# Performance work log

Hardware: AMD Instinct MI355X
Metric: run time of the kernel (lower is better)

The kernel has to match this reference:

```python
import jax, jax.numpy as jnp
import numpy as np

D = 512      # dgm / hidden width
L = 3        # n_dgm_layers
B = 131072   # collocation batch
SCALE = 0.02 # init scale to keep gates unsaturated


def setup_inputs() -> dict:
    key = jax.random.key(0)
    ks = jax.random.split(key, 12)
    X = jax.random.normal(ks[0], (B, 2), jnp.float32)
    t = jax.random.uniform(ks[1], (B, 1), jnp.float32)
    # input layer: Linear(3, D)
    W_in = jax.random.normal(ks[2], (3, D), jnp.float32) * SCALE
    b_in = jnp.zeros((D,), jnp.float32)
    # dense hidden: Linear(D, D)
    W_h1 = jax.random.normal(ks[3], (D, D), jnp.float32) * SCALE
    b_h1 = jnp.zeros((D,), jnp.float32)
    # projection to dgm dims: Linear(D, D)
    W_hd = jax.random.normal(ks[4], (D, D), jnp.float32) * SCALE
    b_hd = jnp.zeros((D,), jnp.float32)
    # DGM layers: 12 linears each, order [Uz,Wz,Bz, Ug,Wg,Bg, Ur,Wr,Br, Uh,Wh,Bh]
    dgm_W = jax.random.normal(ks[5], (L, 12, D, D), jnp.float32) * SCALE
    dgm_b = jnp.zeros((L, 12, D), jnp.float32)
    # output head: Linear(D, 1)
    W_out = jax.random.normal(ks[6], (D, 1), jnp.float32) * SCALE
    b_out = jnp.zeros((1,), jnp.float32)
    return {"X": X, "t": t, "W_in": W_in, "b_in": b_in, "W_h1": W_h1,
            "b_h1": b_h1, "W_hd": W_hd, "b_hd": b_hd, "dgm_W": dgm_W,
            "dgm_b": dgm_b, "W_out": W_out, "b_out": b_out}


def reference(X, t, W_in, b_in, W_h1, b_h1, W_hd, b_hd, dgm_W, dgm_b, W_out, b_out):
    inp = jnp.concatenate([X, t], axis=1)          # [B, 3]
    x = jnp.tanh(inp @ W_in + b_in)                # input layer + tanh
    x = jnp.tanh(x @ W_h1 + b_h1)                  # hidden Linear + tanh
    x = x @ W_hd + b_hd                            # hidden -> dgm projection (no act)
    S1 = x
    S = x
    for l in range(L):                             # small fixed layer loop
        W = dgm_W[l]
        b = dgm_b[l]
        lin = lambda i, v: v @ W[i] + b[i]
        Z = jax.nn.sigmoid(lin(0, x) + lin(1, S) + lin(2, S1))
        G = jax.nn.sigmoid(lin(3, x) + lin(4, S1) + lin(5, S))
        R = jax.nn.sigmoid(lin(6, x) + lin(7, S) + lin(8, S1))
        H = jnp.tanh(lin(9, x) + lin(10, S * R) + lin(11, S1))
        S = (1.0 - G) * H + Z * S
    return S @ W_out + b_out                       # [B, 1]
```

## Files before the change

### kernel.cpp

```cpp
#include <hip/hip_runtime.h>
#include <stdint.h>

namespace {

constexpr int B_ROWS = 131072;

typedef __attribute__((ext_vector_type(8))) short bf16x8;
typedef __attribute__((ext_vector_type(4))) float f32x4;

__device__ __forceinline__ unsigned short f2bf(float f) {
  unsigned u = __builtin_bit_cast(unsigned, f);
  u += 0x7fffu + ((u >> 16) & 1u);
  return (unsigned short)(u >> 16);
}
__device__ __forceinline__ float bf2f(unsigned short h) {
  unsigned u = ((unsigned)h) << 16;
  return __builtin_bit_cast(float, u);
}
__device__ __forceinline__ float sigm(float v) { return 1.0f / (1.0f + __expf(-v)); }


__global__ void pack_t_k(const float* __restrict__ W, unsigned short* __restrict__ Wt) {
  int idx = blockIdx.x * 256 + threadIdx.x;
  int n = idx >> 9, k = idx & 511;
  Wt[idx] = f2bf(W[(k << 9) + n]);
}

__global__ void pack_zgr_k(const float* __restrict__ dgmW, unsigned short* __restrict__ Wt) {
  long idx = (long)blockIdx.x * 256 + threadIdx.x;
  int l = (int)(idx / (1536 * 1024));
  int rest = (int)(idx - (long)l * (1536 * 1024));
  int n = rest >> 10, k = rest & 1023;
  int g = n >> 9, nn = n & 511;
  const int xi0[3] = {0, 3, 6};
  const int xi1[3] = {2, 4, 8};
  const int si[3] = {1, 5, 7};
  float v;
  if (k < 512)
    v = dgmW[(((long)(l * 12 + xi0[g]) << 9) + k) * 512 + nn] +
        dgmW[(((long)(l * 12 + xi1[g]) << 9) + k) * 512 + nn];
  else
    v = dgmW[(((long)(l * 12 + si[g]) << 9) + (k - 512)) * 512 + nn];
  Wt[idx] = f2bf(v);
}

__global__ void pack_h_k(const float* __restrict__ dgmW, unsigned short* __restrict__ Wt) {
  long idx = (long)blockIdx.x * 256 + threadIdx.x;
  int l = (int)(idx / (512 * 1024));
  int rest = (int)(idx - (long)l * (512 * 1024));
  int n = rest >> 10, k = rest & 1023;
  float v;
  if (k < 512)
    v = dgmW[(((long)(l * 12 + 9) << 9) + k) * 512 + n] +
        dgmW[(((long)(l * 12 + 11) << 9) + k) * 512 + n];
  else
    v = dgmW[(((long)(l * 12 + 10) << 9) + (k - 512)) * 512 + n];
  Wt[idx] = f2bf(v);
}

__global__ void pack_bias_k(const float* __restrict__ dgmb, float* __restrict__ bzgr,
                            float* __restrict__ bh) {
  int idx = blockIdx.x * 256 + threadIdx.x;
  if (idx >= 3 * 2048) return;
  int l = idx >> 11, n = idx & 2047;
  const float* bl = dgmb + l * 12 * 512;
  if (n < 1536) {
    int g = n >> 9, nn = n & 511;
    bzgr[l * 1536 + n] =
        bl[(g * 3 + 0) * 512 + nn] + bl[(g * 3 + 1) * 512 + nn] + bl[(g * 3 + 2) * 512 + nn];
  } else {
    int nn = n - 1536;
    bh[l * 512 + nn] = bl[9 * 512 + nn] + bl[10 * 512 + nn] + bl[11 * 512 + nn];
  }
}

__global__ void front0_k(const float* __restrict__ X, const float* __restrict__ t,
                         const float* __restrict__ Win, const float* __restrict__ bin,
                         unsigned short* __restrict__ x0, long row0) {
  long idx = (long)blockIdx.x * 256 + threadIdx.x;
  long r = idx >> 9;
  int c = (int)(idx & 511);
  long gr = row0 + r;
  float a = X[gr * 2] * Win[c] + X[gr * 2 + 1] * Win[512 + c] + t[gr] * Win[1024 + c] + bin[c];
  x0[idx] = f2bf(tanhf(a));
}

__global__ void head_k(const unsigned short* __restrict__ S, const float* __restrict__ Wout,
                       const float* __restrict__ bout, float* __restrict__ out, long row0) {
  const int lane = threadIdx.x & 63, wid = threadIdx.x >> 6;
  const long r = (long)blockIdx.x * 4 + wid;
  bf16x8 sv = *(const bf16x8*)&S[r * 512 + lane * 8];
  float sum = 0.f;
#pragma unroll
  for (int i = 0; i < 8; ++i) sum += bf2f((unsigned short)sv[i]) * Wout[lane * 8 + i];
#pragma unroll
  for (int off = 32; off > 0; off >>= 1) sum += __shfl_down(sum, off);
  if (lane == 0) out[row0 + r] = sum + bout[0];
}

template <int EPI, int KTILES>
__global__ __launch_bounds__(256, 2) void gemm_k(
    const unsigned short* __restrict__ a0, const unsigned short* __restrict__ a1,
    const unsigned short* __restrict__ wt, const float* __restrict__ bias,
    unsigned short* __restrict__ o0, unsigned short* __restrict__ o1,
    unsigned short* __restrict__ o2, const unsigned short* __restrict__ e0,
    const unsigned short* __restrict__ e1) {
  constexpr int K = KTILES * 64;
  __shared__ __align__(16) unsigned short As[128 * 64];
  __shared__ __align__(16) unsigned short Bs[128 * 64];
  const int tid = threadIdx.x;
  const int lane = tid & 63;
  const int wid = tid >> 6;
  const int wm = wid >> 1, wn = wid & 1;
  const long brow = (long)blockIdx.y * 128;
  const int bcol = blockIdx.x * 128;
  f32x4 acc[4][4] = {};

  for (int kt = 0; kt < KTILES; ++kt) {
    const unsigned short* asrc = (kt < 8) ? a0 : a1;
    const int kloc = (kt & 7) * 64;
    __syncthreads();
#pragma unroll
    for (int i = 0; i < 4; ++i) {
      const int c = tid + 256 * i;
      const int r = c >> 3, k8 = (c & 7) * 8;
      __builtin_amdgcn_global_load_lds(
          (const __attribute__((address_space(1))) void*)(asrc + (brow + r) * 512 + kloc + k8),
          (__attribute__((address_space(3))) void*)(&As[c * 8]), 16, 0, 0);
      __builtin_amdgcn_global_load_lds(
          (const __attribute__((address_space(1))) void*)(wt + (long)(bcol + r) * K + kt * 64 + k8),
          (__attribute__((address_space(3))) void*)(&Bs[c * 8]), 16, 0, 0);
    }
    __syncthreads();
#pragma unroll
    for (int ks = 0; ks < 2; ++ks) {
      bf16x8 af[4], bfv[4];
#pragma unroll
      for (int m = 0; m < 4; ++m)
        af[m] = *(const bf16x8*)&As[(wm * 64 + m * 16 + (lane & 15)) * 64 + ks * 32 + (lane >> 4) * 8];
#pragma unroll
      for (int n = 0; n < 4; ++n)
        bfv[n] = *(const bf16x8*)&Bs[(wn * 64 + n * 16 + (lane & 15)) * 64 + ks * 32 + (lane >> 4) * 8];
#pragma unroll
      for (int m = 0; m < 4; ++m)
#pragma unroll
        for (int n = 0; n < 4; ++n)
          acc[m][n] = __builtin_amdgcn_mfma_f32_16x16x32_bf16(af[m], bfv[n], acc[m][n], 0, 0, 0);
    }
  }

  const int g = bcol >> 9;
#pragma unroll
  for (int m = 0; m < 4; ++m) {
#pragma unroll
    for (int n = 0; n < 4; ++n) {
      const int col = bcol + wn * 64 + n * 16 + (lane & 15);
      const float bs = bias[col];
#pragma unroll
      for (int j = 0; j < 4; ++j) {
        const long row = brow + wm * 64 + m * 16 + (lane >> 4) * 4 + j;
        float v = acc[m][n][j] + bs;
        if constexpr (EPI == 0) {
          o0[row * 512 + col] = f2bf(tanhf(v));
        } else if constexpr (EPI == 1) {
          unsigned short b = f2bf(v);
          o0[row * 512 + col] = b;
          o1[row * 512 + col] = b;
        } else if constexpr (EPI == 2) {
          const int nn = col & 511;
          const float sgv = sigm(v);
          if (g == 0) {
            o0[row * 512 + nn] = f2bf(sgv * bf2f(e0[row * 512 + nn]));
          } else if (g == 1) {
            o1[row * 512 + nn] = f2bf(1.0f - sgv);
          } else {
            o2[row * 512 + nn] = f2bf(sgv * bf2f(e0[row * 512 + nn]));
          }
        } else {
          const float h = tanhf(v);
          const float omg = bf2f(e0[row * 512 + col]);
          const float zs = bf2f(e1[row * 512 + col]);
          o0[row * 512 + col] = f2bf(omg * h + zs);
        }
      }
    }
  }
}

}

extern "C" void kernel_launch(void* const* d_in, const int* in_sizes, int n_in,
                              void* d_out, int out_size, void* d_ws, size_t ws_size,
                              hipStream_t stream) {
  const float* X = (const float*)d_in[0];
  const float* t = (const float*)d_in[1];
  const float* W_in = (const float*)d_in[2];
  const float* b_in = (const float*)d_in[3];
  const float* W_h1 = (const float*)d_in[4];
  const float* b_h1 = (const float*)d_in[5];
  const float* W_hd = (const float*)d_in[6];
  const float* b_hd = (const float*)d_in[7];
  const float* dgm_W = (const float*)d_in[8];
  const float* dgm_b = (const float*)d_in[9];
  const float* W_out = (const float*)d_in[10];
  const float* b_out = (const float*)d_in[11];
  float* out = (float*)d_out;
  char* ws = (char*)d_ws;

  size_t off = 0;
  auto alloc = [&](size_t bytes) {
    size_t o = off;
    off = (off + bytes + 255) & ~(size_t)255;
    return o;
  };
  size_t o_wth1 = alloc((size_t)512 * 512 * 2);
  size_t o_wthd = alloc((size_t)512 * 512 * 2);
  size_t o_wtzgr = alloc((size_t)3 * 1536 * 1024 * 2);
  size_t o_wth = alloc((size_t)3 * 512 * 1024 * 2);
  size_t o_bzgr = alloc((size_t)3 * 1536 * 4);
  size_t o_bh = alloc((size_t)3 * 512 * 4);
  size_t actoff = off;

  unsigned short* wth1 = (unsigned short*)(ws + o_wth1);
  unsigned short* wthd = (unsigned short*)(ws + o_wthd);
  unsigned short* wtzgr = (unsigned short*)(ws + o_wtzgr);
  unsigned short* wth = (unsigned short*)(ws + o_wth);
  float* bzgr = (float*)(ws + o_bzgr);
  float* bh = (float*)(ws + o_bh);

  size_t avail = ws_size > actoff ? ws_size - actoff : 0;
  int nch = 1;
  while (nch < 1024 && (size_t)(B_ROWS / nch) * 512 * 2 * 5 > avail) nch <<= 1;
  const int R = B_ROWS / nch;
  unsigned short* xb = (unsigned short*)(ws + actoff);
  unsigned short* Sb = xb + (size_t)R * 512;
  unsigned short* ZSb = Sb + (size_t)R * 512;
  unsigned short* OGb = ZSb + (size_t)R * 512;
  unsigned short* SRb = OGb + (size_t)R * 512;

  pack_t_k<<<1024, 256, 0, stream>>>(W_h1, wth1);
  pack_t_k<<<1024, 256, 0, stream>>>(W_hd, wthd);
  pack_zgr_k<<<18432, 256, 0, stream>>>(dgm_W, wtzgr);
  pack_h_k<<<6144, 256, 0, stream>>>(dgm_W, wth);
  pack_bias_k<<<24, 256, 0, stream>>>(dgm_b, bzgr, bh);

  for (int c = 0; c < nch; ++c) {
    long row0 = (long)c * R;
    dim3 g4(4, R / 128), g12(12, R / 128);
    front0_k<<<R * 2, 256, 0, stream>>>(X, t, W_in, b_in, ZSb, row0);
    gemm_k<0, 8><<<g4, 256, 0, stream>>>(ZSb, nullptr, wth1, b_h1, OGb, nullptr, nullptr,
                                         nullptr, nullptr);
    gemm_k<1, 8><<<g4, 256, 0, stream>>>(OGb, nullptr, wthd, b_hd, xb, Sb, nullptr,
                                         nullptr, nullptr);
    for (int l = 0; l < 3; ++l) {
      gemm_k<2, 16><<<g12, 256, 0, stream>>>(xb, Sb, wtzgr + (size_t)l * 1536 * 1024,
                                             bzgr + l * 1536, ZSb, OGb, SRb, Sb, nullptr);
      gemm_k<3, 16><<<g4, 256, 0, stream>>>(xb, SRb, wth + (size_t)l * 512 * 1024,
                                            bh + l * 512, Sb, nullptr, nullptr, OGb, ZSb);
    }
    head_k<<<R / 4, 256, 0, stream>>>(Sb, W_out, b_out, out, row0);
  }
}
```

Baseline: 3.627 ms.

## Rewrite GEMM with 256x256 tiles, double-buffered swizzled LDS and XCD remap

Replaces the 128x128, 256-thread GEMM with a 512-thread kernel that computes 256x256 output tiles. It uses 128KB of dynamic LDS split into two buffers, so the next K-tile is prefetched while MFMAs run on the current one. LDS rows are XOR-swizzled to avoid bank conflicts, workgroups are remapped so neighbouring tiles land on the same XCD, and s_setprio is raised around the MFMA block. The larger tile raises arithmetic intensity per load, at the cost of one block per CU, heavy register use and a requirement that the chunk row count be a multiple of 256.

```diff
diff --git a/kernel.cpp b/kernel.cpp
--- a/kernel.cpp
+++ b/kernel.cpp
@@ -98,67 +98,107 @@
   if (lane == 0) out[row0 + r] = sum + bout[0];
 }
 
-template <int EPI, int KTILES>
-__global__ __launch_bounds__(256, 2) void gemm_k(
+#define GLD(gsrc, ldst)                                                      \
+  __builtin_amdgcn_global_load_lds(                                          \
+      (const __attribute__((address_space(1))) void*)(gsrc),                 \
+      (__attribute__((address_space(3))) void*)(ldst), 16, 0, 0)
+
+template <int EPI, int KT>
+__global__ __launch_bounds__(512, 2) void gemm2_k(
     const unsigned short* __restrict__ a0, const unsigned short* __restrict__ a1,
     const unsigned short* __restrict__ wt, const float* __restrict__ bias,
     unsigned short* __restrict__ o0, unsigned short* __restrict__ o1,
     unsigned short* __restrict__ o2, const unsigned short* __restrict__ e0,
     const unsigned short* __restrict__ e1) {
-  constexpr int K = KTILES * 64;
-  __shared__ __align__(16) unsigned short As[128 * 64];
-  __shared__ __align__(16) unsigned short Bs[128 * 64];
+  constexpr int K = KT * 64;
+  extern __shared__ unsigned short lds[];
   const int tid = threadIdx.x;
-  const int lane = tid & 63;
-  const int wid = tid >> 6;
-  const int wm = wid >> 1, wn = wid & 1;
-  const long brow = (long)blockIdx.y * 128;
-  const int bcol = blockIdx.x * 128;
-  f32x4 acc[4][4] = {};
-
-  for (int kt = 0; kt < KTILES; ++kt) {
-    const unsigned short* asrc = (kt < 8) ? a0 : a1;
-    const int kloc = (kt & 7) * 64;
+  const int lane = tid & 63, wid = tid >> 6;
+  const int wm = wid >> 2, wn = wid & 3;
+  const int lr = lane & 15, kk = lane >> 4;
+
+  const int gx = gridDim.x;
+  const int nwg = gx * (int)gridDim.y;
+  const int orig = (int)blockIdx.y * gx + (int)blockIdx.x;
+  const int q = nwg >> 3, rr = nwg & 7;
+  const int xcd = orig & 7, lo = orig >> 3;
+  const int wg = ((xcd < rr) ? xcd * (q + 1) : rr * (q + 1) + (xcd - rr) * q) + lo;
+  const long brow = (long)(wg / gx) * 256;
+  const int bcol = (wg % gx) * 256;
+
+  const int gp8 = ((kk ^ ((lr >> 1) & 3)) << 3);
+  const int a_rd = (wm * 128 + lr) * 32 + gp8;
+  const int b_rd = 16384 + (wn * 64 + lr) * 32 + gp8;
+  const int r0 = tid >> 2, gl0 = (tid & 3) ^ ((r0 >> 1) & 3);
+  const int c1t = tid + 512, r1 = c1t >> 2, gl1 = (c1t & 3) ^ ((r1 >> 1) & 3);
+  const int aL0 = r0 * 512 + gl0 * 8, aL1 = r1 * 512 + gl1 * 8;
+  const size_t bL0 = (size_t)r0 * K + gl0 * 8, bL1 = (size_t)r1 * K + gl1 * 8;
+  const int dL0 = tid * 8, dL1 = (tid + 512) * 8;
+
+  f32x4 acc[8][4] = {};
+  bf16x8 af[8], bf[4];
+
+  const long abase = brow * 512;
+  const size_t bbase = (size_t)bcol * K;
+
+  auto stA = [&](int kt, int ks, int dbo) {
+    const unsigned short* src = (KT == 16 && (kt & 8)) ? a1 : a0;
+    const long pb = abase + (kt & 7) * 64 + ks * 32;
+    const int d = dbo + ks * 8192;
+    GLD(src + pb + aL0, lds + d + dL0);
+    GLD(src + pb + aL1, lds + d + dL1);
+  };
+  auto stB = [&](int kt, int ks, int dbo) {
+    const size_t pb = bbase + kt * 64 + ks * 32;
+    const int d = dbo + 16384 + ks * 8192;
+    GLD(wt + pb + bL0, lds + d + dL0);
+    GLD(wt + pb + bL1, lds + d + dL1);
+  };
+
+  stA(0, 0, 0);
+  stB(0, 0, 0);
+  stA(0, 1, 0);
+  stB(0, 1, 0);
+  asm volatile("s_waitcnt vmcnt(0)" ::: "memory");
+  __syncthreads();
+
+  for (int t = 0; t < KT; ++t) {
+    const int cbo = (t & 1) << 15;
+    const int nbo = cbo ^ 32768;
+    if (t + 1 < KT) {
+      stA(t + 1, 0, nbo);
+      stB(t + 1, 0, nbo);
+      stA(t + 1, 1, nbo);
+      stB(t + 1, 1, nbo);
+    }
+#pragma unroll
+    for (int ks = 0; ks < 2; ++ks) {
+      const int ko = cbo + ks * 8192;
+#pragma unroll
+      for (int n = 0; n < 4; ++n) bf[n] = *(const bf16x8*)(lds + ko + b_rd + n * 512);
+#pragma unroll
+      for (int m = 0; m < 8; ++m) af[m] = *(const bf16x8*)(lds + ko + a_rd + m * 512);
+      __builtin_amdgcn_s_setprio(1);
+#pragma unroll
+      for (int m = 0; m < 8; ++m)
+#pragma unroll
+        for (int n = 0; n < 4; ++n)
+          acc[m][n] = __builtin_amdgcn_mfma_f32_16x16x32_bf16(af[m], bf[n], acc[m][n], 0, 0, 0);
+      __builtin_amdgcn_s_setprio(0);
+    }
+    asm volatile("s_waitcnt vmcnt(0)" ::: "memory");
     __syncthreads();
-#pragma unroll
-    for (int i = 0; i < 4; ++i) {
-      const int c = tid + 256 * i;
-      const int r = c >> 3, k8 = (c & 7) * 8;
-      __builtin_amdgcn_global_load_lds(
-          (const __attribute__((address_space(1))) void*)(asrc + (brow + r) * 512 + kloc + k8),
-          (__attribute__((address_space(3))) void*)(&As[c * 8]), 16, 0, 0);
-      __builtin_amdgcn_global_load_lds(
-          (const __attribute__((address_space(1))) void*)(wt + (long)(bcol + r) * K + kt * 64 + k8),
-          (__attribute__((address_space(3))) void*)(&Bs[c * 8]), 16, 0, 0);
-    }
-    __syncthreads();
-#pragma unroll
-    for (int ks = 0; ks < 2; ++ks) {
-      bf16x8 af[4], bfv[4];
-#pragma unroll
-      for (int m = 0; m < 4; ++m)
-        af[m] = *(const bf16x8*)&As[(wm * 64 + m * 16 + (lane & 15)) * 64 + ks * 32 + (lane >> 4) * 8];
-#pragma unroll
-      for (int n = 0; n < 4; ++n)
-        bfv[n] = *(const bf16x8*)&Bs[(wn * 64 + n * 16 + (lane & 15)) * 64 + ks * 32 + (lane >> 4) * 8];
-#pragma unroll
-      for (int m = 0; m < 4; ++m)
-#pragma unroll
-        for (int n = 0; n < 4; ++n)
-          acc[m][n] = __builtin_amdgcn_mfma_f32_16x16x32_bf16(af[m], bfv[n], acc[m][n], 0, 0, 0);
-    }
   }
 
-  const int g = bcol >> 9;
-#pragma unroll
-  for (int m = 0; m < 4; ++m) {
+#pragma unroll
+  for (int m = 0; m < 8; ++m) {
 #pragma unroll
     for (int n = 0; n < 4; ++n) {
-      const int col = bcol + wn * 64 + n * 16 + (lane & 15);
+      const int col = bcol + wn * 64 + n * 16 + lr;
       const float bs = bias[col];
 #pragma unroll
       for (int j = 0; j < 4; ++j) {
-        const long row = brow + wm * 64 + m * 16 + (lane >> 4) * 4 + j;
+        const long row = brow + wm * 128 + m * 16 + kk * 4 + j;
         float v = acc[m][n][j] + bs;
         if constexpr (EPI == 0) {
           o0[row * 512 + col] = f2bf(tanhf(v));
@@ -167,6 +207,7 @@
           o0[row * 512 + col] = b;
           o1[row * 512 + col] = b;
         } else if constexpr (EPI == 2) {
+          const int g = col >> 9;
           const int nn = col & 511;
           const float sgv = sigm(v);
           if (g == 0) {
@@ -207,6 +248,15 @@
   float* out = (float*)d_out;
   char* ws = (char*)d_ws;
 
+  (void)hipFuncSetAttribute((const void*)&gemm2_k<0, 8>,
+                            hipFuncAttributeMaxDynamicSharedMemorySize, 131072);
+  (void)hipFuncSetAttribute((const void*)&gemm2_k<1, 8>,
+                            hipFuncAttributeMaxDynamicSharedMemorySize, 131072);
+  (void)hipFuncSetAttribute((const void*)&gemm2_k<2, 16>,
+                            hipFuncAttributeMaxDynamicSharedMemorySize, 131072);
+  (void)hipFuncSetAttribute((const void*)&gemm2_k<3, 16>,
+                            hipFuncAttributeMaxDynamicSharedMemorySize, 131072);
+
   size_t off = 0;
   auto alloc = [&](size_t bytes) {
     size_t o = off;
@@ -230,7 +280,7 @@
 
   size_t avail = ws_size > actoff ? ws_size - actoff : 0;
   int nch = 1;
-  while (nch < 1024 && (size_t)(B_ROWS / nch) * 512 * 2 * 5 > avail) nch <<= 1;
+  while (nch < 256 && (size_t)(B_ROWS / nch) * 512 * 2 * 5 > avail) nch <<= 1;
   const int R = B_ROWS / nch;
   unsigned short* xb = (unsigned short*)(ws + actoff);
   unsigned short* Sb = xb + (size_t)R * 512;
@@ -244,19 +294,20 @@
   pack_h_k<<<6144, 256, 0, stream>>>(dgm_W, wth);
   pack_bias_k<<<24, 256, 0, stream>>>(dgm_b, bzgr, bh);
 
+  const int MT = R / 256;
   for (int c = 0; c < nch; ++c) {
     long row0 = (long)c * R;
-    dim3 g4(4, R / 128), g12(12, R / 128);
+    dim3 g2(2, MT), g6(6, MT);
     front0_k<<<R * 2, 256, 0, stream>>>(X, t, W_in, b_in, ZSb, row0);
-    gemm_k<0, 8><<<g4, 256, 0, stream>>>(ZSb, nullptr, wth1, b_h1, OGb, nullptr, nullptr,
-                                         nullptr, nullptr);
-    gemm_k<1, 8><<<g4, 256, 0, stream>>>(OGb, nullptr, wthd, b_hd, xb, Sb, nullptr,
-                                         nullptr, nullptr);
+    gemm2_k<0, 8><<<g2, 512, 131072, stream>>>(ZSb, ZSb, wth1, b_h1, OGb, nullptr, nullptr,
+                                               nullptr, nullptr);
+    gemm2_k<1, 8><<<g2, 512, 131072, stream>>>(OGb, OGb, wthd, b_hd, xb, Sb, nullptr,
+                                               nullptr, nullptr);
     for (int l = 0; l < 3; ++l) {
-      gemm_k<2, 16><<<g12, 256, 0, stream>>>(xb, Sb, wtzgr + (size_t)l * 1536 * 1024,
-                                             bzgr + l * 1536, ZSb, OGb, SRb, Sb, nullptr);
-      gemm_k<3, 16><<<g4, 256, 0, stream>>>(xb, SRb, wth + (size_t)l * 512 * 1024,
-                                            bh + l * 512, Sb, nullptr, nullptr, OGb, ZSb);
+      gemm2_k<2, 16><<<g6, 512, 131072, stream>>>(xb, Sb, wtzgr + (size_t)l * 1536 * 1024,
+                                                  bzgr + l * 1536, ZSb, OGb, SRb, Sb, nullptr);
+      gemm2_k<3, 16><<<g2, 512, 131072, stream>>>(xb, SRb, wth + (size_t)l * 512 * 1024,
+                                                  bh + l * 512, Sb, nullptr, nullptr, OGb, ZSb);
     }
     head_k<<<R / 4, 256, 0, stream>>>(Sb, W_out, b_out, out, row0);
   }
```

Measured after the change: 3.385 ms. 1.07x faster.

## Narrow GEMM tiles to 128x64 with swizzled LDS, XCD remap and higher occupancy

Applied to the files above, without the earlier changes.

Replaces the 128x128 GEMM tile with a 128x64 tile that uses a single 24 KB LDS buffer, so launch bounds can ask for 4 workgroups per CU instead of 2. It XOR-swizzles the LDS layout to cut bank conflicts on fragment reads and remaps workgroup IDs so that neighbouring tiles land on the same XCD for better L2 reuse. MFMA issue is wrapped in s_setprio. The grids double in the N dimension and the chunk-count cap drops. In exchange, each A tile is loaded twice as often per output, which raises global and L2 traffic per FLOP.

```diff
diff --git a/kernel.cpp b/kernel.cpp
--- a/kernel.cpp
+++ b/kernel.cpp
@@ -98,67 +98,92 @@
   if (lane == 0) out[row0 + r] = sum + bout[0];
 }
 
-template <int EPI, int KTILES>
-__global__ __launch_bounds__(256, 2) void gemm_k(
+#define GLD(gsrc, ldst)                                                      \
+  __builtin_amdgcn_global_load_lds(                                          \
+      (const __attribute__((address_space(1))) void*)(gsrc),                 \
+      (__attribute__((address_space(3))) void*)(ldst), 16, 0, 0)
+
+template <int EPI, int KT>
+__global__ __launch_bounds__(256, 4) void gemmS_k(
     const unsigned short* __restrict__ a0, const unsigned short* __restrict__ a1,
     const unsigned short* __restrict__ wt, const float* __restrict__ bias,
     unsigned short* __restrict__ o0, unsigned short* __restrict__ o1,
     unsigned short* __restrict__ o2, const unsigned short* __restrict__ e0,
     const unsigned short* __restrict__ e1) {
-  constexpr int K = KTILES * 64;
-  __shared__ __align__(16) unsigned short As[128 * 64];
-  __shared__ __align__(16) unsigned short Bs[128 * 64];
+  constexpr int K = KT * 64;
+  __shared__ unsigned short lds[12288];
   const int tid = threadIdx.x;
-  const int lane = tid & 63;
-  const int wid = tid >> 6;
+  const int lane = tid & 63, wid = tid >> 6;
   const int wm = wid >> 1, wn = wid & 1;
-  const long brow = (long)blockIdx.y * 128;
-  const int bcol = blockIdx.x * 128;
-  f32x4 acc[4][4] = {};
-
-  for (int kt = 0; kt < KTILES; ++kt) {
-    const unsigned short* asrc = (kt < 8) ? a0 : a1;
-    const int kloc = (kt & 7) * 64;
+  const int lr = lane & 15, kk = lane >> 4;
+
+  const int gx = gridDim.x;
+  const int nwg = gx * (int)gridDim.y;
+  const int orig = (int)blockIdx.y * gx + (int)blockIdx.x;
+  const int q = nwg >> 3, rr = nwg & 7;
+  const int xcd = orig & 7, lo = orig >> 3;
+  const int wg = ((xcd < rr) ? xcd * (q + 1) : rr * (q + 1) + (xcd - rr) * q) + lo;
+  const long brow = (long)(wg / gx) * 128;
+  const int bcol = (wg % gx) * 64;
+
+  const int gp8 = ((kk ^ ((lr >> 1) & 3)) << 3);
+  const int a_rd = (wm * 64 + lr) * 32 + gp8;
+  const int b_rd = 8192 + (wn * 32 + lr) * 32 + gp8;
+
+  f32x4 acc[4][2] = {};
+
+  auto stage = [&](int kt) {
+    const unsigned short* src = (KT == 16 && (kt & 8)) ? a1 : a0;
+    const int ko = (kt & 7) * 64;
+#pragma unroll
+    for (int i = 0; i < 4; ++i) {
+      const int u = tid + (i << 8);
+      const int ks = u >> 9, rem = u & 511;
+      const int row = rem >> 2;
+      const int gl = (rem & 3) ^ ((row >> 1) & 3);
+      GLD(src + (brow + row) * 512 + ko + ks * 32 + gl * 8, lds + u * 8);
+    }
+#pragma unroll
+    for (int i = 0; i < 2; ++i) {
+      const int u = tid + (i << 8);
+      const int ks = u >> 8, rem = u & 255;
+      const int row = rem >> 2;
+      const int gl = (rem & 3) ^ ((row >> 1) & 3);
+      GLD(wt + (size_t)(bcol + row) * K + kt * 64 + ks * 32 + gl * 8, lds + 8192 + u * 8);
+    }
+  };
+
+  for (int t = 0; t < KT; ++t) {
     __syncthreads();
-#pragma unroll
-    for (int i = 0; i < 4; ++i) {
-      const int c = tid + 256 * i;
-      const int r = c >> 3, k8 = (c & 7) * 8;
-      __builtin_amdgcn_global_load_lds(
-          (const __attribute__((address_space(1))) void*)(asrc + (brow + r) * 512 + kloc + k8),
-          (__attribute__((address_space(3))) void*)(&As[c * 8]), 16, 0, 0);
-      __builtin_amdgcn_global_load_lds(
-          (const __attribute__((address_space(1))) void*)(wt + (long)(bcol + r) * K + kt * 64 + k8),
-          (__attribute__((address_space(3))) void*)(&Bs[c * 8]), 16, 0, 0);
-    }
+    stage(t);
     __syncthreads();
 #pragma unroll
     for (int ks = 0; ks < 2; ++ks) {
-      bf16x8 af[4], bfv[4];
+      bf16x8 bf0 = *(const bf16x8*)(lds + b_rd + ks * 2048);
+      bf16x8 bf1 = *(const bf16x8*)(lds + b_rd + ks * 2048 + 512);
+      bf16x8 af[4];
 #pragma unroll
       for (int m = 0; m < 4; ++m)
-        af[m] = *(const bf16x8*)&As[(wm * 64 + m * 16 + (lane & 15)) * 64 + ks * 32 + (lane >> 4) * 8];
-#pragma unroll
-      for (int n = 0; n < 4; ++n)
-        bfv[n] = *(const bf16x8*)&Bs[(wn * 64 + n * 16 + (lane & 15)) * 64 + ks * 32 + (lane >> 4) * 8];
-#pragma unroll
-      for (int m = 0; m < 4; ++m)
-#pragma unroll
-        for (int n = 0; n < 4; ++n)
-          acc[m][n] = __builtin_amdgcn_mfma_f32_16x16x32_bf16(af[m], bfv[n], acc[m][n], 0, 0, 0);
-    }
-  }
-
-  const int g = bcol >> 9;
+        af[m] = *(const bf16x8*)(lds + a_rd + ks * 4096 + m * 512);
+      __builtin_amdgcn_s_setprio(1);
+#pragma unroll
+      for (int m = 0; m < 4; ++m) {
+        acc[m][0] = __builtin_amdgcn_mfma_f32_16x16x32_bf16(af[m], bf0, acc[m][0], 0, 0, 0);
+        acc[m][1] = __builtin_amdgcn_mfma_f32_16x16x32_bf16(af[m], bf1, acc[m][1], 0, 0, 0);
+      }
+      __builtin_amdgcn_s_setprio(0);
+    }
+  }
+
 #pragma unroll
   for (int m = 0; m < 4; ++m) {
 #pragma unroll
-    for (int n = 0; n < 4; ++n) {
-      const int col = bcol + wn * 64 + n * 16 + (lane & 15);
+    for (int n = 0; n < 2; ++n) {
+      const int col = bcol + wn * 32 + n * 16 + lr;
       const float bs = bias[col];
 #pragma unroll
       for (int j = 0; j < 4; ++j) {
-        const long row = brow + wm * 64 + m * 16 + (lane >> 4) * 4 + j;
+        const long row = brow + wm * 64 + m * 16 + kk * 4 + j;
         float v = acc[m][n][j] + bs;
         if constexpr (EPI == 0) {
           o0[row * 512 + col] = f2bf(tanhf(v));
@@ -167,6 +192,7 @@
           o0[row * 512 + col] = b;
           o1[row * 512 + col] = b;
         } else if constexpr (EPI == 2) {
+          const int g = col >> 9;
           const int nn = col & 511;
           const float sgv = sigm(v);
           if (g == 0) {
@@ -230,7 +256,7 @@
 
   size_t avail = ws_size > actoff ? ws_size - actoff : 0;
   int nch = 1;
-  while (nch < 1024 && (size_t)(B_ROWS / nch) * 512 * 2 * 5 > avail) nch <<= 1;
+  while (nch < 256 && (size_t)(B_ROWS / nch) * 512 * 2 * 5 > avail) nch <<= 1;
   const int R = B_ROWS / nch;
   unsigned short* xb = (unsigned short*)(ws + actoff);
   unsigned short* Sb = xb + (size_t)R * 512;
@@ -244,19 +270,20 @@
   pack_h_k<<<6144, 256, 0, stream>>>(dgm_W, wth);
   pack_bias_k<<<24, 256, 0, stream>>>(dgm_b, bzgr, bh);
 
+  const int MT = R / 128;
   for (int c = 0; c < nch; ++c) {
     long row0 = (long)c * R;
-    dim3 g4(4, R / 128), g12(12, R / 128);
+    dim3 g8(8, MT), g24(24, MT);
     front0_k<<<R * 2, 256, 0, stream>>>(X, t, W_in, b_in, ZSb, row0);
-    gemm_k<0, 8><<<g4, 256, 0, stream>>>(ZSb, nullptr, wth1, b_h1, OGb, nullptr, nullptr,
-                                         nullptr, nullptr);
-    gemm_k<1, 8><<<g4, 256, 0, stream>>>(OGb, nullptr, wthd, b_hd, xb, Sb, nullptr,
-                                         nullptr, nullptr);
+    gemmS_k<0, 8><<<g8, 256, 0, stream>>>(ZSb, ZSb, wth1, b_h1, OGb, nullptr, nullptr,
+                                          nullptr, nullptr);
+    gemmS_k<1, 8><<<g8, 256, 0, stream>>>(OGb, OGb, wthd, b_hd, xb, Sb, nullptr,
+                                          nullptr, nullptr);
     for (int l = 0; l < 3; ++l) {
-      gemm_k<2, 16><<<g12, 256, 0, stream>>>(xb, Sb, wtzgr + (size_t)l * 1536 * 1024,
-                                             bzgr + l * 1536, ZSb, OGb, SRb, Sb, nullptr);
-      gemm_k<3, 16><<<g4, 256, 0, stream>>>(xb, SRb, wth + (size_t)l * 512 * 1024,
-                                            bh + l * 512, Sb, nullptr, nullptr, OGb, ZSb);
+      gemmS_k<2, 16><<<g24, 256, 0, stream>>>(xb, Sb, wtzgr + (size_t)l * 1536 * 1024,
+                                              bzgr + l * 1536, ZSb, OGb, SRb, Sb, nullptr);
+      gemmS_k<3, 16><<<g8, 256, 0, stream>>>(xb, SRb, wth + (size_t)l * 512 * 1024,
+                                             bh + l * 512, Sb, nullptr, nullptr, OGb, ZSb);
     }
     head_k<<<R / 4, 256, 0, stream>>>(Sb, W_out, b_out, out, row0);
   }
```

After: 3.013 ms. -16.9%, faster.
